# Kernel optimization log

Measured on AMD Instinct MI355X. Metric: run time of the kernel, lower is better.

## Reference

```python
import jax, jax.numpy as jnp
import numpy as np
jax.config.update("jax_enable_x64", True)

MAX_DEPTH = 21
SENTINEL = np.int64(2 ** 62)  # pads invalid (consumed) slots; > any real morton code


def split_by3(n):
    n = n & 2097151
    n = (n | (n << 32)) & 8725724278095871
    n = (n | (n << 16)) & 8725728556220671
    n = (n | (n << 8)) & 1157144660301377551
    n = (n | (n << 4)) & 1207822528635744451
    n = (n | (n << 2)) & 1317624576693539401
    return n


def _unique_agg(codes, feats):
    # codes: [N] sorted int64 (SENTINEL-padded at the end); feats: [N, F]
    # Emulates torch.unique_consecutive + scatter_add with fixed shapes.
    N = codes.shape[0]
    is_new = jnp.concatenate([jnp.ones((1,), dtype=bool), codes[1:] != codes[:-1]])
    seg = jnp.cumsum(is_new) - 1  # consecutive-group id (reverse index)
    agg = jax.ops.segment_sum(feats, seg, num_segments=N)
    ucodes = jnp.full((N,), SENTINEL, dtype=jnp.int64).at[seg].set(codes)
    count = jnp.sum(is_new & (codes != SENTINEL)).astype(jnp.int32)
    return ucodes, agg, count


def setup_inputs() -> dict:
    key = jax.random.key(0)
    N = 262144
    new_cloud = jax.random.normal(key, (N, 4), dtype=jnp.float32)
    leaf_size = jnp.full((3,), 0.1, dtype=jnp.float32)
    return {"new_cloud": new_cloud, "leaf_size": leaf_size}


def reference(new_cloud, leaf_size):
    xyz = new_cloud[:, :3]
    n = new_cloud.shape[0]
    # aggregated features: [count=1, xyz, xyz^2, extra cols]
    feats = jnp.concatenate(
        [jnp.ones((n, 1), new_cloud.dtype), xyz, xyz * xyz, new_cloud[:, 3:]], axis=1
    )
    origin = jnp.min(xyz, axis=0) - 0.5 * leaf_size
    ijk = jnp.floor((xyz - origin) / leaf_size).astype(jnp.int64)
    s = split_by3(ijk)
    codes = s[:, 0] | (s[:, 1] << 1) | (s[:, 2] << 2)
    order = jnp.argsort(codes)
    codes = codes[order]
    feats = feats[order]
    mc, ag, cnt = _unique_agg(codes, feats)
    mcs, ags, cnts = [mc], [ag], [cnt]
    for d in range(1, MAX_DEPTH):
        shifted = jnp.where(mc == SENTINEL, SENTINEL, mc >> 3)
        mc, ag, cnt = _unique_agg(shifted, ag)
        mcs.append(mc)
        ags.append(ag)
        cnts.append(cnt)
    # [MAX_DEPTH, N] codes (SENTINEL-padded), [MAX_DEPTH, N, F] aggregates (zero-padded), [MAX_DEPTH] valid counts
    return jnp.stack(mcs), jnp.stack(ags), jnp.stack(cnts)
```

## Files before the change

kernel.cpp:

```cpp
#include <hip/hip_runtime.h>
#include <stdint.h>

static constexpr int L0N = 2097152;
static constexpr int O1 = 0;
static constexpr int O2 = 262144, S2 = 32768;
static constexpr int O3 = 294912, S3 = 4096;
static constexpr int O4 = 299008, S4 = 512;
static constexpr int O5 = 300032, S5 = 64;
static constexpr int O6 = 301056, S6 = 8;
static constexpr int O7 = 302080;
static constexpr int UP_TOT = 303104;
static constexpr int UNBLK = 296;

__device__ __forceinline__ unsigned s3_rB(unsigned n){
  n &= 0x3FFu;
  n = (n | (n << 16)) & 0x030000FFu;
  n = (n | (n << 8))  & 0x0300F00Fu;
  n = (n | (n << 4))  & 0x030C30C3u;
  n = (n | (n << 2))  & 0x09249249u;
  return n;
}

__device__ __forceinline__ unsigned long long packE(unsigned st, unsigned c, unsigned f){
  return ((unsigned long long)st << 62) | ((unsigned long long)c << 21) | (unsigned long long)f;
}

__device__ __forceinline__ int block_scan_incl(int v, int tid, int* total){
  __shared__ int w4[4];
  __syncthreads();
  int lane = tid & 63, wid = tid >> 6;
  #pragma unroll
  for (int o = 1; o < 64; o <<= 1){
    int n = __shfl_up(v, o, 64);
    if (lane >= o) v += n;
  }
  if (lane == 63) w4[wid] = v;
  __syncthreads();
  if (tid < 4){
    int w = w4[tid];
    #pragma unroll
    for (int o = 1; o < 4; o <<= 1){
      int n = __shfl_up(w, o, 4);
      if (tid >= o) w += n;
    }
    w4[tid] = w;
  }
  __syncthreads();
  if (wid > 0) v += w4[wid - 1];
  *total = w4[3];
  return v;
}

__device__ __forceinline__ void grid_spin_barrier(int* ctr, int nblocks){
  __threadfence();
  __syncthreads();
  if (threadIdx.x == 0){
    atomicAdd(ctr, 1);
    while (atomicAdd(ctr, 0) < nblocks) ;
  }
  __syncthreads();
  __threadfence();
}

__device__ __forceinline__ void wave_block_min3(float& mx, float& my, float& mz, int tid){
  #pragma unroll
  for (int o = 32; o; o >>= 1){
    mx = fminf(mx, __shfl_down(mx, o, 64));
    my = fminf(my, __shfl_down(my, o, 64));
    mz = fminf(mz, __shfl_down(mz, o, 64));
  }
  __shared__ float sm[3][4];
  int lane = tid & 63, wid = tid >> 6;
  if (lane == 0){ sm[0][wid] = mx; sm[1][wid] = my; sm[2][wid] = mz; }
  __syncthreads();
  if (tid == 0){
    for (int w = 1; w < 4; w++){
      mx = fminf(mx, sm[0][w]); my = fminf(my, sm[1][w]); mz = fminf(mz, sm[2][w]);
    }
  }
}

__global__ void kminzero_rB(const float4* __restrict__ cloud, int n,
                            int* __restrict__ C0, int* __restrict__ aux, int auxN,
                            float* __restrict__ pmins){
  int gid = blockIdx.x * blockDim.x + threadIdx.x;
  int gstride = gridDim.x * blockDim.x;
  int4 z = {0,0,0,0};
  for (int v = gid; v < L0N / 4; v += gstride)
    ((int4*)C0)[v] = z;
  if (gid < auxN) aux[gid] = 0;
  float mx = INFINITY, my = INFINITY, mz = INFINITY;
  for (int i = gid; i < n; i += gstride){
    float4 p = cloud[i];
    mx = fminf(mx, p.x); my = fminf(my, p.y); mz = fminf(mz, p.z);
  }
  wave_block_min3(mx, my, mz, threadIdx.x);
  if (threadIdx.x == 0){
    pmins[3 * blockIdx.x + 0] = mx;
    pmins[3 * blockIdx.x + 1] = my;
    pmins[3 * blockIdx.x + 2] = mz;
  }
}

__global__ __launch_bounds__(256, 4)
void kA_rB(const float4* __restrict__ cloud, const float* __restrict__ leaf,
           const float* __restrict__ pmins, unsigned* __restrict__ mA, int n,
           int* __restrict__ C0, int2* __restrict__ CR){
  int t = threadIdx.x;
  if (blockIdx.x == 0){
    float mx = pmins[3 * t + 0];
    float my = pmins[3 * t + 1];
    float mz = pmins[3 * t + 2];
    wave_block_min3(mx, my, mz, t);
    if (t == 0){
      atomicExch(&mA[0], __float_as_uint(mx));
      atomicExch(&mA[1], __float_as_uint(my));
      atomicExch(&mA[2], __float_as_uint(mz));
      __threadfence();
      atomicExch(&mA[3], 1u);
    }
  }
  __shared__ float sox, soy, soz, slx, sly, slz;
  if (t == 0){
    while (atomicAdd(&mA[3], 0u) == 0u) ;
    __threadfence();
    float lx = leaf[0], ly = leaf[1], lz = leaf[2];
    slx = lx; sly = ly; slz = lz;
    sox = __uint_as_float(atomicAdd(&mA[0], 0u)) - 0.5f * lx;
    soy = __uint_as_float(atomicAdd(&mA[1], 0u)) - 0.5f * ly;
    soz = __uint_as_float(atomicAdd(&mA[2], 0u)) - 0.5f * lz;
  }
  __syncthreads();
  int i = blockIdx.x * 256 + t;
  if (i >= n) return;
  float4 p = cloud[i];
  int ix = (int)floorf((p.x - sox) / slx);
  int iy = (int)floorf((p.y - soy) / sly);
  int iz = (int)floorf((p.z - soz) / slz);
  ix = min(max(ix, 0), 127); iy = min(max(iy, 0), 127); iz = min(max(iz, 0), 127);
  int code = (int)(s3_rB((unsigned)ix) | (s3_rB((unsigned)iy) << 1) | (s3_rB((unsigned)iz) << 2));
  int rank = atomicAdd(C0 + code, 1);
  CR[i] = {code, rank};
}

__global__ __launch_bounds__(256, 4)
void kscanE_rB(const int* __restrict__ C0, int* __restrict__ E,
               int* __restrict__ flagBase, unsigned long long* __restrict__ statusE,
               float* __restrict__ cnts){
  int b = blockIdx.x, t = threadIdx.x;
  const int4* c4 = (const int4*)(C0 + (size_t)b * 2048 + t * 8);
  int4 a = c4[0], d = c4[1];
  int k[8] = {a.x, a.y, a.z, a.w, d.x, d.y, d.z, d.w};
  int cs = 0, fs = 0;
  #pragma unroll
  for (int c = 0; c < 8; c++){ cs += k[c]; fs += (k[c] != 0); }
  int cTot, fTot;
  int ic = block_scan_incl(cs, t, &cTot);
  block_scan_incl(fs, t, &fTot);
  if (t == 0)
    atomicExch(&statusE[b], packE(b == 0 ? 2u : 1u, (unsigned)cTot, (unsigned)fTot));
  __shared__ unsigned eCs, eFs;
  if (b == 0){
    if (t == 0){ eCs = 0; eFs = 0; }
  } else if (t < 64){
    unsigned sum_c = 0, sum_f = 0;
    int offset = 0;
    bool done = false;
    while (!done){
      int idx = b - 1 - offset - t;
      unsigned long long v = 0;
      unsigned st = 2;
      if (idx >= 0){
        do { v = atomicAdd(&statusE[idx], 0ULL); st = (unsigned)(v >> 62); } while (st == 0);
      }
      unsigned long long m2 = __ballot(st == 2);
      if (m2){
        int f2 = __ffsll((unsigned long long)m2) - 1;
        if (t <= f2){ sum_c += (unsigned)((v >> 21) & 0x1FFFFFu); sum_f += (unsigned)(v & 0x1FFFFFu); }
        done = true;
      } else {
        sum_c += (unsigned)((v >> 21) & 0x1FFFFFu); sum_f += (unsigned)(v & 0x1FFFFFu);
        offset += 64;
      }
    }
    #pragma unroll
    for (int o = 32; o; o >>= 1){
      sum_c += __shfl_down(sum_c, o, 64);
      sum_f += __shfl_down(sum_f, o, 64);
    }
    if (t == 0){
      eCs = sum_c; eFs = sum_f;
      atomicExch(&statusE[b], packE(2u, sum_c + (unsigned)cTot, sum_f + (unsigned)fTot));
    }
  }
  __syncthreads();
  unsigned eC = eCs, eF = eFs;
  if (t == 0){
    flagBase[b] = (int)eF;
    if (b == 1023) cnts[0] = (float)(eF + (unsigned)fTot);
  }
  int e = (int)eC + (ic - cs);
  int ev[8];
  #pragma unroll
  for (int c = 0; c < 8; c++){ ev[c] = e; e += k[c]; }
  int4* e4 = (int4*)(E + (size_t)b * 2048 + t * 8);
  e4[0] = {ev[0], ev[1], ev[2], ev[3]};
  e4[1] = {ev[4], ev[5], ev[6], ev[7]};
}

__global__ __launch_bounds__(256, 4)
void kplace_rB(const float4* __restrict__ cloud, const int2* __restrict__ CR,
               const int* __restrict__ E, int n, float4* __restrict__ S){
  int i = blockIdx.x * blockDim.x + threadIdx.x;
  if (i >= n) return;
  int2 cr = CR[i];
  S[E[cr.x] + cr.y] = cloud[i];
}

__global__ __launch_bounds__(256, 4)
void kbuild1f_rB(const float4* __restrict__ S, const int* __restrict__ C0,
                 const int* __restrict__ E, const int* __restrict__ flagBase,
                 float* __restrict__ PU, int* __restrict__ CU,
                 float* __restrict__ out, int N){
  int b = blockIdx.x, t = threadIdx.x;
  int i = b * 256 + t;
  int s0 = 8 * i;
  const int4* c4 = (const int4*)(C0 + s0);
  int4 ca = c4[0], cb = c4[1];
  int k[8] = {ca.x, ca.y, ca.z, ca.w, cb.x, cb.y, cb.z, cb.w};
  const int4* e4 = (const int4*)(E + s0);
  int4 ea = e4[0], eb = e4[1];
  int eo[8] = {ea.x, ea.y, ea.z, ea.w, eb.x, eb.y, eb.z, eb.w};
  int fs = 0;
  #pragma unroll
  for (int c = 0; c < 8; c++) fs += (k[c] != 0);
  int tot;
  int incl = block_scan_incl(fs, t, &tot);
  int pos = flagBase[b] + (incl - fs);
  size_t MCS = (size_t)21 * N;
  float4 pa = {0,0,0,0}, pb = {0,0,0,0};
  #pragma unroll
  for (int c = 0; c < 8; c++){
    if (k[c] > 0){
      float4 a = {0,0,0,0}, bb = {0,0,0,0};
      int base = eo[c];
      for (int j = 0; j < k[c]; j++){
        float4 pt = S[base + j];
        a.x += 1.0f;        a.y += pt.x;        a.z += pt.y;        a.w += pt.z;
        bb.x += pt.x*pt.x;  bb.y += pt.y*pt.y;  bb.z += pt.z*pt.z;  bb.w += pt.w;
      }
      out[pos] = (float)(s0 + c);
      float4* ag = (float4*)(out + MCS + (size_t)pos * 8);
      ag[0] = a; ag[1] = bb;
      pos++;
      pa.x += a.x; pa.y += a.y; pa.z += a.z; pa.w += a.w;
      pb.x += bb.x; pb.y += bb.y; pb.z += bb.z; pb.w += bb.w;
    }
  }
  float4* prec = (float4*)(PU + (size_t)i * 8);
  prec[0] = pa; prec[1] = pb;
  CU[i] = (int)pa.x;
}

__device__ __forceinline__ void build_one_rB(float* __restrict__ PU, int* __restrict__ CU,
                                             int srcOff, int dstOff, int p){
  const float4* s = (const float4*)(PU + (size_t)(srcOff + 8 * p) * 8);
  float4 a = {0,0,0,0}, b = {0,0,0,0};
  #pragma unroll
  for (int c = 0; c < 8; c++){
    float4 u = s[2 * c], v = s[2 * c + 1];
    a.x += u.x; a.y += u.y; a.z += u.z; a.w += u.w;
    b.x += v.x; b.y += v.y; b.z += v.z; b.w += v.w;
  }
  float4* d = (float4*)(PU + (size_t)(dstOff + p) * 8);
  d[0] = a; d[1] = b;
  CU[dstOff + p] = (int)a.x;
}

__global__ __launch_bounds__(256, 4)
void kbuildUp_rB(float* __restrict__ PU, int* __restrict__ CU, int* __restrict__ ctrs){
  int b = blockIdx.x, t = threadIdx.x;
  build_one_rB(PU, CU, O1, O2, b * 256 + t);
  grid_spin_barrier(&ctrs[0], 128);
  if (t < 32) build_one_rB(PU, CU, O2, O3, b * 32 + t);
  grid_spin_barrier(&ctrs[1], 128);
  if (b != 0) return;
  for (int i2 = O4 + S4 + t; i2 < UP_TOT; i2 += 256) CU[i2] = 0;
  __syncthreads();
  for (int p = t; p < S4; p += 256) build_one_rB(PU, CU, O3, O4, p);
  __syncthreads();
  if (t < S5) build_one_rB(PU, CU, O4, O5, t);
  __syncthreads();
  if (t < S6) build_one_rB(PU, CU, O5, O6, t);
  __syncthreads();
  if (t == 0) build_one_rB(PU, CU, O6, O7, 0);
}

__global__ __launch_bounds__(256, 4)
void kscanU_rB(const float* __restrict__ PU, const int* __restrict__ CU,
               unsigned long long* __restrict__ statusU,
               float* __restrict__ out, float* __restrict__ cnts, int N){
  int b = blockIdx.x, t = threadIdx.x;
  size_t MCS = (size_t)21 * N;
  if (b == UNBLK){
    if (t < 104){
      int dd = 8 + (t >> 3), q = t & 7;
      out[MCS + ((size_t)dd * N) * 8 + q] = PU[(size_t)O7 * 8 + q];
    } else if (t < 117){
      int dd = 8 + (t - 104);
      out[(size_t)dd * N] = 0.0f;
    }
    return;
  }
  int lvl, soff, segStart, lastTile;
  if      (b < 256){ lvl = 1; soff = O1; segStart = 0;   lastTile = 255; }
  else if (b < 288){ lvl = 2; soff = O2; segStart = 256; lastTile = 287; }
  else if (b < 292){ lvl = 3; soff = O3; segStart = 288; lastTile = 291; }
  else if (b < 293){ lvl = 4; soff = O4; segStart = 292; lastTile = 292; }
  else if (b < 294){ lvl = 5; soff = O5; segStart = 293; lastTile = 293; }
  else if (b < 295){ lvl = 6; soff = O6; segStart = 294; lastTile = 294; }
  else             { lvl = 7; soff = O7; segStart = 295; lastTile = 295; }
  int slot0 = b * 1024 + t * 4;
  int4 v = ((const int4*)CU)[(size_t)b * 256 + t];
  int fl[4] = { v.x != 0, v.y != 0, v.z != 0, v.w != 0 };
  int c = fl[0] + fl[1] + fl[2] + fl[3];
  int tot;
  int incl = block_scan_incl(c, t, &tot);
  if (t == 0)
    atomicExch(&statusU[b], ((unsigned long long)(b == segStart ? 2u : 1u) << 62)
                            | (unsigned long long)(unsigned)tot);
  __shared__ unsigned eFs;
  if (b == segStart){
    if (t == 0) eFs = 0;
  } else if (t < 64){
    unsigned sum_f = 0;
    int offset = 0;
    bool done = false;
    while (!done){
      int idx = b - 1 - offset - t;
      unsigned long long vv = 0;
      unsigned st = 2;
      if (idx >= segStart){
        do { vv = atomicAdd(&statusU[idx], 0ULL); st = (unsigned)(vv >> 62); } while (st == 0);
      }
      unsigned long long m2 = __ballot(st == 2);
      if (m2){
        int f2 = __ffsll((unsigned long long)m2) - 1;
        if (t <= f2) sum_f += (unsigned)(vv & 0x3FFFFFFFu);
        done = true;
      } else {
        sum_f += (unsigned)(vv & 0x3FFFFFFFu);
        offset += 64;
      }
    }
    #pragma unroll
    for (int o = 32; o; o >>= 1) sum_f += __shfl_down(sum_f, o, 64);
    if (t == 0){
      eFs = sum_f;
      atomicExch(&statusU[b], (2ULL << 62) | (unsigned long long)(sum_f + (unsigned)tot));
    }
  }
  __syncthreads();
  int p = (int)eFs + (incl - c);
  if (t == 0 && b == lastTile){
    float total = (float)(eFs + (unsigned)tot);
    if (lvl < 7) cnts[lvl] = total;
    else { for (int dd = 7; dd < 21; dd++) cnts[dd] = total; }
  }
  #pragma unroll
  for (int kk = 0; kk < 4; kk++){
    if (fl[kk]){
      int slot = slot0 + kk;
      out[(size_t)lvl * N + p] = (float)(slot - soff);
      const float4* rec = (const float4*)(PU + (size_t)slot * 8);
      float4* ag = (float4*)(out + MCS + ((size_t)lvl * N + p) * 8);
      ag[0] = rec[0]; ag[1] = rec[1];
      p++;
    }
  }
}

extern "C" void kernel_launch(void* const* d_in, const int* in_sizes, int n_in,
                              void* d_out, int out_size, void* d_ws, size_t ws_size,
                              hipStream_t stream){
  int ci = 0, li = 1;
  if (n_in >= 2 && in_sizes[0] == 3){ ci = 1; li = 0; }
  const float4* cloud = (const float4*)d_in[ci];
  const float*  leaf  = (const float*)d_in[li];
  int N = in_sizes[ci] / 4;

  float* out = (float*)d_out;
  float* PU   = (float*)d_ws;
  int*   C0   = (int*)(PU + (size_t)UP_TOT * 8);
  int*   CU   = C0 + L0N;
  int*   E    = CU + UP_TOT;
  int2*  CR   = (int2*)(E + L0N);
  float4* S   = (float4*)(CR + N);
  unsigned long long* statusE = (unsigned long long*)(S + N);
  unsigned long long* statusU = statusE + 1024;
  int* flagBase = (int*)(statusU + 512);
  int* ctrs     = flagBase + 1024;
  unsigned* mA  = (unsigned*)(ctrs + 4);
  float* pmins  = (float*)(mA + 4);
  int* auxZero  = (int*)statusE;
  int auxN      = 2048 + 1024 + 1024 + 4 + 4;
  float* cnts   = out + (size_t)189 * N;

  kminzero_rB<<<256, 256, 0, stream>>>(cloud, N, C0, auxZero, auxN, pmins);
  kA_rB<<<(N + 255) / 256, 256, 0, stream>>>(cloud, leaf, pmins, mA, N, C0, CR);
  kscanE_rB<<<1024, 256, 0, stream>>>(C0, E, flagBase, statusE, cnts);
  kplace_rB<<<(N + 255) / 256, 256, 0, stream>>>(cloud, CR, E, N, S);
  kbuild1f_rB<<<1024, 256, 0, stream>>>(S, C0, E, flagBase, PU, CU, out, N);
  kbuildUp_rB<<<128, 256, 0, stream>>>(PU, CU, &ctrs[0]);
  kscanU_rB<<<UNBLK + 1, 256, 0, stream>>>(PU, CU, statusU, out, cnts, N);
}
```

Before: 362.9 us.

## Fuse upper-level build into scan kernel and use scoped acquire/release atomics

Merges the upper octree level build kernel and the upper-level compaction scan into one 297-block kernel, separated by three agent-scope grid barriers, which removes one kernel launch. The spin loops and status publishing switch from atomicAdd/atomicExch polling with full threadfences to agent-scoped relaxed, acquire and release loads and stores with s_sleep backoff, aiming to cut atomic traffic and fence cost. The grid barrier assumes all 297 blocks are resident at once. The decoupled-lookback status words are now stored relaxed without an explicit fence, which weakens ordering.

```diff
diff --git a/kernel.cpp b/kernel.cpp
--- a/kernel.cpp
+++ b/kernel.cpp
@@ -12,7 +12,9 @@
 static constexpr int UP_TOT = 303104;
 static constexpr int UNBLK = 296;
 
-__device__ __forceinline__ unsigned s3_rB(unsigned n){
+#define AGENT __HIP_MEMORY_SCOPE_AGENT
+
+__device__ __forceinline__ unsigned s3_rC(unsigned n){
   n &= 0x3FFu;
   n = (n | (n << 16)) & 0x030000FFu;
   n = (n | (n << 8))  & 0x0300F00Fu;
@@ -51,15 +53,14 @@
   return v;
 }
 
-__device__ __forceinline__ void grid_spin_barrier(int* ctr, int nblocks){
-  __threadfence();
+__device__ __forceinline__ void grid_bar(int* ctr, int target){
   __syncthreads();
   if (threadIdx.x == 0){
-    atomicAdd(ctr, 1);
-    while (atomicAdd(ctr, 0) < nblocks) ;
-  }
-  __syncthreads();
-  __threadfence();
+    __hip_atomic_fetch_add(ctr, 1, __ATOMIC_ACQ_REL, AGENT);
+    while (__hip_atomic_load(ctr, __ATOMIC_ACQUIRE, AGENT) < target)
+      __builtin_amdgcn_s_sleep(2);
+  }
+  __syncthreads();
 }
 
 __device__ __forceinline__ void wave_block_min3(float& mx, float& my, float& mz, int tid){
@@ -80,7 +81,7 @@
   }
 }
 
-__global__ void kminzero_rB(const float4* __restrict__ cloud, int n,
+__global__ void kminzero_rC(const float4* __restrict__ cloud, int n,
                             int* __restrict__ C0, int* __restrict__ aux, int auxN,
                             float* __restrict__ pmins){
   int gid = blockIdx.x * blockDim.x + threadIdx.x;
@@ -103,7 +104,7 @@
 }
 
 __global__ __launch_bounds__(256, 4)
-void kA_rB(const float4* __restrict__ cloud, const float* __restrict__ leaf,
+void kA_rC(const float4* __restrict__ cloud, const float* __restrict__ leaf,
            const float* __restrict__ pmins, unsigned* __restrict__ mA, int n,
            int* __restrict__ C0, int2* __restrict__ CR){
   int t = threadIdx.x;
@@ -113,22 +114,21 @@
     float mz = pmins[3 * t + 2];
     wave_block_min3(mx, my, mz, t);
     if (t == 0){
-      atomicExch(&mA[0], __float_as_uint(mx));
-      atomicExch(&mA[1], __float_as_uint(my));
-      atomicExch(&mA[2], __float_as_uint(mz));
-      __threadfence();
-      atomicExch(&mA[3], 1u);
+      __hip_atomic_store(&mA[0], __float_as_uint(mx), __ATOMIC_RELAXED, AGENT);
+      __hip_atomic_store(&mA[1], __float_as_uint(my), __ATOMIC_RELAXED, AGENT);
+      __hip_atomic_store(&mA[2], __float_as_uint(mz), __ATOMIC_RELAXED, AGENT);
+      __hip_atomic_store(&mA[3], 1u, __ATOMIC_RELEASE, AGENT);
     }
   }
   __shared__ float sox, soy, soz, slx, sly, slz;
   if (t == 0){
-    while (atomicAdd(&mA[3], 0u) == 0u) ;
-    __threadfence();
+    while (__hip_atomic_load(&mA[3], __ATOMIC_ACQUIRE, AGENT) == 0u)
+      __builtin_amdgcn_s_sleep(1);
     float lx = leaf[0], ly = leaf[1], lz = leaf[2];
     slx = lx; sly = ly; slz = lz;
-    sox = __uint_as_float(atomicAdd(&mA[0], 0u)) - 0.5f * lx;
-    soy = __uint_as_float(atomicAdd(&mA[1], 0u)) - 0.5f * ly;
-    soz = __uint_as_float(atomicAdd(&mA[2], 0u)) - 0.5f * lz;
+    sox = __uint_as_float(__hip_atomic_load(&mA[0], __ATOMIC_RELAXED, AGENT)) - 0.5f * lx;
+    soy = __uint_as_float(__hip_atomic_load(&mA[1], __ATOMIC_RELAXED, AGENT)) - 0.5f * ly;
+    soz = __uint_as_float(__hip_atomic_load(&mA[2], __ATOMIC_RELAXED, AGENT)) - 0.5f * lz;
   }
   __syncthreads();
   int i = blockIdx.x * 256 + t;
@@ -138,13 +138,13 @@
   int iy = (int)floorf((p.y - soy) / sly);
   int iz = (int)floorf((p.z - soz) / slz);
   ix = min(max(ix, 0), 127); iy = min(max(iy, 0), 127); iz = min(max(iz, 0), 127);
-  int code = (int)(s3_rB((unsigned)ix) | (s3_rB((unsigned)iy) << 1) | (s3_rB((unsigned)iz) << 2));
+  int code = (int)(s3_rC((unsigned)ix) | (s3_rC((unsigned)iy) << 1) | (s3_rC((unsigned)iz) << 2));
   int rank = atomicAdd(C0 + code, 1);
   CR[i] = {code, rank};
 }
 
 __global__ __launch_bounds__(256, 4)
-void kscanE_rB(const int* __restrict__ C0, int* __restrict__ E,
+void kscanE_rC(const int* __restrict__ C0, int* __restrict__ E,
                int* __restrict__ flagBase, unsigned long long* __restrict__ statusE,
                float* __restrict__ cnts){
   int b = blockIdx.x, t = threadIdx.x;
@@ -158,7 +158,8 @@
   int ic = block_scan_incl(cs, t, &cTot);
   block_scan_incl(fs, t, &fTot);
   if (t == 0)
-    atomicExch(&statusE[b], packE(b == 0 ? 2u : 1u, (unsigned)cTot, (unsigned)fTot));
+    __hip_atomic_store(&statusE[b], packE(b == 0 ? 2u : 1u, (unsigned)cTot, (unsigned)fTot),
+                       __ATOMIC_RELAXED, AGENT);
   __shared__ unsigned eCs, eFs;
   if (b == 0){
     if (t == 0){ eCs = 0; eFs = 0; }
@@ -171,7 +172,12 @@
       unsigned long long v = 0;
       unsigned st = 2;
       if (idx >= 0){
-        do { v = atomicAdd(&statusE[idx], 0ULL); st = (unsigned)(v >> 62); } while (st == 0);
+        for (;;){
+          v = __hip_atomic_load(&statusE[idx], __ATOMIC_RELAXED, AGENT);
+          st = (unsigned)(v >> 62);
+          if (st) break;
+          __builtin_amdgcn_s_sleep(1);
+        }
       }
       unsigned long long m2 = __ballot(st == 2);
       if (m2){
@@ -190,7 +196,8 @@
     }
     if (t == 0){
       eCs = sum_c; eFs = sum_f;
-      atomicExch(&statusE[b], packE(2u, sum_c + (unsigned)cTot, sum_f + (unsigned)fTot));
+      __hip_atomic_store(&statusE[b], packE(2u, sum_c + (unsigned)cTot, sum_f + (unsigned)fTot),
+                         __ATOMIC_RELAXED, AGENT);
     }
   }
   __syncthreads();
@@ -209,7 +216,7 @@
 }
 
 __global__ __launch_bounds__(256, 4)
-void kplace_rB(const float4* __restrict__ cloud, const int2* __restrict__ CR,
+void kplace_rC(const float4* __restrict__ cloud, const int2* __restrict__ CR,
                const int* __restrict__ E, int n, float4* __restrict__ S){
   int i = blockIdx.x * blockDim.x + threadIdx.x;
   if (i >= n) return;
@@ -218,7 +225,7 @@
 }
 
 __global__ __launch_bounds__(256, 4)
-void kbuild1f_rB(const float4* __restrict__ S, const int* __restrict__ C0,
+void kbuild1f_rC(const float4* __restrict__ S, const int* __restrict__ C0,
                  const int* __restrict__ E, const int* __restrict__ flagBase,
                  float* __restrict__ PU, int* __restrict__ CU,
                  float* __restrict__ out, int N){
@@ -262,7 +269,7 @@
   CU[i] = (int)pa.x;
 }
 
-__device__ __forceinline__ void build_one_rB(float* __restrict__ PU, int* __restrict__ CU,
+__device__ __forceinline__ void build_one_rC(float* __restrict__ PU, int* __restrict__ CU,
                                              int srcOff, int dstOff, int p){
   const float4* s = (const float4*)(PU + (size_t)(srcOff + 8 * p) * 8);
   float4 a = {0,0,0,0}, b = {0,0,0,0};
@@ -278,29 +285,28 @@
 }
 
 __global__ __launch_bounds__(256, 4)
-void kbuildUp_rB(float* __restrict__ PU, int* __restrict__ CU, int* __restrict__ ctrs){
-  int b = blockIdx.x, t = threadIdx.x;
-  build_one_rB(PU, CU, O1, O2, b * 256 + t);
-  grid_spin_barrier(&ctrs[0], 128);
-  if (t < 32) build_one_rB(PU, CU, O2, O3, b * 32 + t);
-  grid_spin_barrier(&ctrs[1], 128);
-  if (b != 0) return;
-  for (int i2 = O4 + S4 + t; i2 < UP_TOT; i2 += 256) CU[i2] = 0;
-  __syncthreads();
-  for (int p = t; p < S4; p += 256) build_one_rB(PU, CU, O3, O4, p);
-  __syncthreads();
-  if (t < S5) build_one_rB(PU, CU, O4, O5, t);
-  __syncthreads();
-  if (t < S6) build_one_rB(PU, CU, O5, O6, t);
-  __syncthreads();
-  if (t == 0) build_one_rB(PU, CU, O6, O7, 0);
-}
-
-__global__ __launch_bounds__(256, 4)
-void kscanU_rB(const float* __restrict__ PU, const int* __restrict__ CU,
+void kupper_rC(float* __restrict__ PU, int* __restrict__ CU, int* __restrict__ ctrs,
                unsigned long long* __restrict__ statusU,
                float* __restrict__ out, float* __restrict__ cnts, int N){
   int b = blockIdx.x, t = threadIdx.x;
+  const int NB = 297;
+  if (b < 128) build_one_rC(PU, CU, O1, O2, b * 256 + t);
+  grid_bar(&ctrs[0], NB);
+  if (b < 16)  build_one_rC(PU, CU, O2, O3, b * 256 + t);
+  grid_bar(&ctrs[1], NB);
+  if (b == 0){
+    for (int i2 = O4 + S4 + t; i2 < UP_TOT; i2 += 256) CU[i2] = 0;
+    __syncthreads();
+    for (int p = t; p < S4; p += 256) build_one_rC(PU, CU, O3, O4, p);
+    __syncthreads();
+    if (t < S5) build_one_rC(PU, CU, O4, O5, t);
+    __syncthreads();
+    if (t < S6) build_one_rC(PU, CU, O5, O6, t);
+    __syncthreads();
+    if (t == 0) build_one_rC(PU, CU, O6, O7, 0);
+  }
+  grid_bar(&ctrs[2], NB);
+
   size_t MCS = (size_t)21 * N;
   if (b == UNBLK){
     if (t < 104){
@@ -327,8 +333,9 @@
   int tot;
   int incl = block_scan_incl(c, t, &tot);
   if (t == 0)
-    atomicExch(&statusU[b], ((unsigned long long)(b == segStart ? 2u : 1u) << 62)
-                            | (unsigned long long)(unsigned)tot);
+    __hip_atomic_store(&statusU[b],
+        ((unsigned long long)(b == segStart ? 2u : 1u) << 62) | (unsigned long long)(unsigned)tot,
+        __ATOMIC_RELAXED, AGENT);
   __shared__ unsigned eFs;
   if (b == segStart){
     if (t == 0) eFs = 0;
@@ -341,7 +348,12 @@
       unsigned long long vv = 0;
       unsigned st = 2;
       if (idx >= segStart){
-        do { vv = atomicAdd(&statusU[idx], 0ULL); st = (unsigned)(vv >> 62); } while (st == 0);
+        for (;;){
+          vv = __hip_atomic_load(&statusU[idx], __ATOMIC_RELAXED, AGENT);
+          st = (unsigned)(vv >> 62);
+          if (st) break;
+          __builtin_amdgcn_s_sleep(1);
+        }
       }
       unsigned long long m2 = __ballot(st == 2);
       if (m2){
@@ -357,7 +369,9 @@
     for (int o = 32; o; o >>= 1) sum_f += __shfl_down(sum_f, o, 64);
     if (t == 0){
       eFs = sum_f;
-      atomicExch(&statusU[b], (2ULL << 62) | (unsigned long long)(sum_f + (unsigned)tot));
+      __hip_atomic_store(&statusU[b],
+          (2ULL << 62) | (unsigned long long)(sum_f + (unsigned)tot),
+          __ATOMIC_RELAXED, AGENT);
     }
   }
   __syncthreads();
@@ -400,17 +414,16 @@
   unsigned long long* statusU = statusE + 1024;
   int* flagBase = (int*)(statusU + 512);
   int* ctrs     = flagBase + 1024;
-  unsigned* mA  = (unsigned*)(ctrs + 4);
+  unsigned* mA  = (unsigned*)(ctrs + 8);
   float* pmins  = (float*)(mA + 4);
   int* auxZero  = (int*)statusE;
-  int auxN      = 2048 + 1024 + 1024 + 4 + 4;
+  int auxN      = 2048 + 1024 + 1024 + 8 + 4;
   float* cnts   = out + (size_t)189 * N;
 
-  kminzero_rB<<<256, 256, 0, stream>>>(cloud, N, C0, auxZero, auxN, pmins);
-  kA_rB<<<(N + 255) / 256, 256, 0, stream>>>(cloud, leaf, pmins, mA, N, C0, CR);
-  kscanE_rB<<<1024, 256, 0, stream>>>(C0, E, flagBase, statusE, cnts);
-  kplace_rB<<<(N + 255) / 256, 256, 0, stream>>>(cloud, CR, E, N, S);
-  kbuild1f_rB<<<1024, 256, 0, stream>>>(S, C0, E, flagBase, PU, CU, out, N);
-  kbuildUp_rB<<<128, 256, 0, stream>>>(PU, CU, &ctrs[0]);
-  kscanU_rB<<<UNBLK + 1, 256, 0, stream>>>(PU, CU, statusU, out, cnts, N);
-}
+  kminzero_rC<<<256, 256, 0, stream>>>(cloud, N, C0, auxZero, auxN, pmins);
+  kA_rC<<<(N + 255) / 256, 256, 0, stream>>>(cloud, leaf, pmins, mA, N, C0, CR);
+  kscanE_rC<<<1024, 256, 0, stream>>>(C0, E, flagBase, statusE, cnts);
+  kplace_rC<<<(N + 255) / 256, 256, 0, stream>>>(cloud, CR, E, N, S);
+  kbuild1f_rC<<<1024, 256, 0, stream>>>(S, C0, E, flagBase, PU, CU, out, N);
+  kupper_rC<<<UNBLK + 1, 256, 0, stream>>>(PU, CU, ctrs, statusU, out, cnts, N);
+}
```

After: 444.7 us. 1.23x slower.
